# Kernel tuning notes

Hardware: AMD Instinct MI355X
Metric: run time of the kernel (lower is better)

The kernel has to match this reference:

```python
import jax, jax.numpy as jnp
import numpy as np

TOP_K = 2

def setup_inputs() -> dict:
    key = jax.random.key(0)
    k1, k2 = jax.random.split(key)
    x = jax.random.normal(k1, (4, 4096, 4096), dtype=jnp.float32)
    # nn.Linear(hidden, experts, bias=False) weight: [num_experts, hidden]
    gate_w = jax.random.normal(k2, (64, 4096), dtype=jnp.float32) * (1.0 / np.sqrt(4096.0))
    return {"x": x, "gate_w": gate_w}

def reference(x, gate_w):
    # logits: [b, s, e] = x @ gate_w.T
    logits = jnp.einsum('bsh,eh->bse', x, gate_w)
    top_k_logits, top_k_indices = jax.lax.top_k(logits, TOP_K)  # [b, s, k]
    # softmax over top-k logits in float32, cast back to logits dtype
    probs = jax.nn.softmax(top_k_logits.astype(jnp.float32), axis=-1).astype(logits.dtype)
    return (logits, top_k_indices, probs)
```

## Files before the change

kernel.cpp:

```cpp
#include <hip/hip_runtime.h>
#include <math.h>

#define H 4096
#define E 64
#define BMROWS 32
#define NT 256
#define KQ 1024
#define BK 32
#define NWIN (KQ / BK)

typedef short bf16x8 __attribute__((ext_vector_type(8)));
typedef float f32x4  __attribute__((ext_vector_type(4)));

__device__ __forceinline__ unsigned f2bf_rne_u(float f) {
    unsigned u = __float_as_uint(f);
    return (u + 0x7fffu + ((u >> 16) & 1u)) >> 16;
}

__global__ __launch_bounds__(256) void convert_w(const float* __restrict__ w,
                                                 unsigned short* __restrict__ wh,
                                                 unsigned short* __restrict__ wl) {
    const int i = (blockIdx.x * 256 + threadIdx.x) * 4;
    float4 v = *(const float4*)(w + i);
    float vv[4] = {v.x, v.y, v.z, v.w};
    unsigned hh[4], ll[4];
#pragma unroll
    for (int j = 0; j < 4; ++j) {
        hh[j] = f2bf_rne_u(vv[j]);
        float r = vv[j] - __uint_as_float(hh[j] << 16);
        ll[j] = __float_as_uint(r) >> 16;
    }
    ushort4 h, l;
    h.x = (unsigned short)hh[0]; h.y = (unsigned short)hh[1];
    h.z = (unsigned short)hh[2]; h.w = (unsigned short)hh[3];
    l.x = (unsigned short)ll[0]; l.y = (unsigned short)ll[1];
    l.z = (unsigned short)ll[2]; l.w = (unsigned short)ll[3];
    *(ushort4*)(wh + i) = h;
    *(ushort4*)(wl + i) = l;
}

__device__ __forceinline__ void cvt8(const float4 a, const float4 b,
                                     bf16x8& hi, bf16x8& lo) {
    float v[8] = {a.x, a.y, a.z, a.w, b.x, b.y, b.z, b.w};
#pragma unroll
    for (int i = 0; i < 8; ++i) {
        const unsigned u = __float_as_uint(v[i]);
        const unsigned t = u + 0x7fffu + ((u >> 16) & 1u);
        const float    r = v[i] - __uint_as_float(t & 0xffff0000u);
        hi[i] = (short)(t >> 16);
        lo[i] = (short)(__float_as_uint(r) >> 16);
    }
}

__global__ __launch_bounds__(NT, 2) void router_kernel(
    const float* __restrict__ x,
    const unsigned short* __restrict__ wh,
    const unsigned short* __restrict__ wl,
    float* __restrict__ out, int M)
{
    __shared__ __align__(16) f32x4 merge[8][4][64];

    const int t    = threadIdx.x;
    const int lane = t & 63;
    const int wk   = t >> 6;
    const int m0   = blockIdx.x * BMROWS;
    const int col  = lane & 15;
    const int quad = lane >> 4;

    const int kbase = wk * KQ + quad * 8;

    const float* xp0 = x + (size_t)(m0 + col) * H + kbase;
    const float* xp1 = x + (size_t)(m0 + 16 + col) * H + kbase;
    const unsigned short* whp = wh + (size_t)col * H + kbase;
    const unsigned short* wlp = wl + (size_t)col * H + kbase;

    f32x4 acc[2][4];
#pragma unroll
    for (int mt = 0; mt < 2; ++mt)
#pragma unroll
        for (int nt = 0; nt < 4; ++nt)
            acc[mt][nt] = (f32x4){0.0f, 0.0f, 0.0f, 0.0f};

    float4 x0[2][2], x1[2][2], x2[2][2], x3[2][2];
    uint4  wAh[4], wAl[4], wBh[4], wBl[4];

    auto loadx_into = [&](int win, float4 (&xb)[2][2]) {
        const int k = win * BK;
        xb[0][0] = *(const float4*)(xp0 + k);
        xb[0][1] = *(const float4*)(xp0 + k + 4);
        xb[1][0] = *(const float4*)(xp1 + k);
        xb[1][1] = *(const float4*)(xp1 + k + 4);
    };
    auto loadw_into = [&](int win, uint4 (&wh_)[4], uint4 (&wl_)[4]) {
        const int k = win * BK;
#pragma unroll
        for (int nt = 0; nt < 4; ++nt) {
            wh_[nt] = *(const uint4*)(whp + (size_t)(nt * 16) * H + k);
            wl_[nt] = *(const uint4*)(wlp + (size_t)(nt * 16) * H + k);
        }
    };

    auto step = [&](int win, float4 (&xc)[2][2], float4 (&xpref)[2][2],
                    uint4 (&whc)[4], uint4 (&wlc)[4],
                    uint4 (&whn)[4], uint4 (&wln)[4]) {
        if (win + 3 < NWIN) loadx_into(win + 3, xpref);
        if (win + 1 < NWIN) loadw_into(win + 1, whn, wln);
        bf16x8 ah[2], al[2];
        cvt8(xc[0][0], xc[0][1], ah[0], al[0]);
        cvt8(xc[1][0], xc[1][1], ah[1], al[1]);
#pragma unroll
        for (int nt = 0; nt < 4; ++nt) {
            const bf16x8 bh = __builtin_bit_cast(bf16x8, whc[nt]);
            const bf16x8 bl = __builtin_bit_cast(bf16x8, wlc[nt]);
#pragma unroll
            for (int mt = 0; mt < 2; ++mt) {
                acc[mt][nt] = __builtin_amdgcn_mfma_f32_16x16x32_bf16(
                    ah[mt], bh, acc[mt][nt], 0, 0, 0);
                acc[mt][nt] = __builtin_amdgcn_mfma_f32_16x16x32_bf16(
                    ah[mt], bl, acc[mt][nt], 0, 0, 0);
                acc[mt][nt] = __builtin_amdgcn_mfma_f32_16x16x32_bf16(
                    al[mt], bh, acc[mt][nt], 0, 0, 0);
            }
        }
    };

    loadx_into(0, x0);
    loadx_into(1, x1);
    loadx_into(2, x2);
    loadw_into(0, wAh, wAl);

#pragma unroll 1
    for (int win = 0; win < NWIN; win += 4) {
        step(win,     x0, x3, wAh, wAl, wBh, wBl);
        step(win + 1, x1, x0, wBh, wBl, wAh, wAl);
        step(win + 2, x2, x1, wAh, wAl, wBh, wBl);
        step(win + 3, x3, x2, wBh, wBl, wAh, wAl);
    }

#pragma unroll
    for (int mt = 0; mt < 2; ++mt)
#pragma unroll
        for (int nt = 0; nt < 4; ++nt)
            merge[mt * 4 + nt][wk][lane] = acc[mt][nt];
    __syncthreads();

    if (wk >= 2) return;
    const int mt = wk;

    f32x4 a2[4];
#pragma unroll
    for (int nt = 0; nt < 4; ++nt) {
        f32x4 s = merge[mt * 4 + nt][0][lane];
#pragma unroll
        for (int w = 1; w < 4; ++w)
            s += merge[mt * 4 + nt][w][lane];
        a2[nt] = s;
    }

    float* logits   = out;
    float* idx_out  = out + (size_t)M * E;
    float* prob_out = idx_out + (size_t)M * 2;

    const int mrow = m0 + mt * 16 + quad * 4;
#pragma unroll
    for (int r = 0; r < 4; ++r) {
#pragma unroll
        for (int nt = 0; nt < 4; ++nt)
            logits[(size_t)(mrow + r) * E + nt * 16 + col] = a2[nt][r];

        float v1 = a2[0][r], v2 = -INFINITY;
        int   i1 = col,      i2 = 0x7fffffff;
#pragma unroll
        for (int nt = 1; nt < 4; ++nt) {
            const float v = a2[nt][r];
            const int   e = nt * 16 + col;
            if (v > v1)      { v2 = v1; i2 = i1; v1 = v; i1 = e; }
            else if (v > v2) { v2 = v;  i2 = e; }
        }
#pragma unroll
        for (int mask = 1; mask < 16; mask <<= 1) {
            const float ov1 = __shfl_xor(v1, mask);
            const float ov2 = __shfl_xor(v2, mask);
            const int   oi1 = __shfl_xor(i1, mask);
            const int   oi2 = __shfl_xor(i2, mask);
            const bool afirst = (v1 > ov1) || (v1 == ov1 && i1 < oi1);
            float nv1, nv2; int ni1, ni2;
            if (afirst) {
                nv1 = v1; ni1 = i1;
                const bool s = (v2 > ov1) || (v2 == ov1 && i2 < oi1);
                nv2 = s ? v2 : ov1; ni2 = s ? i2 : oi1;
            } else {
                nv1 = ov1; ni1 = oi1;
                const bool s = (ov2 > v1) || (ov2 == v1 && oi2 < i1);
                nv2 = s ? ov2 : v1; ni2 = s ? oi2 : i1;
            }
            v1 = nv1; v2 = nv2; i1 = ni1; i2 = ni2;
        }
        if (col == 0) {
            const int m = mrow + r;
            const float e2 = __expf(v2 - v1);
            const float d  = 1.0f + e2;
            *(float2*)(idx_out  + (size_t)m * 2) = make_float2((float)i1, (float)i2);
            *(float2*)(prob_out + (size_t)m * 2) = make_float2(1.0f / d, e2 / d);
        }
    }
}

extern "C" void kernel_launch(void* const* d_in, const int* in_sizes, int n_in,
                              void* d_out, int out_size, void* d_ws, size_t ws_size,
                              hipStream_t stream) {
    const float* x = (const float*)d_in[0];
    const float* w = (const float*)d_in[1];
    unsigned short* wh = (unsigned short*)d_ws;
    unsigned short* wl = wh + (size_t)E * H;
    const int M = in_sizes[0] / H;

    hipLaunchKernelGGL(convert_w, dim3((E * H) / 1024), dim3(256), 0, stream,
                       w, wh, wl);
    hipLaunchKernelGGL(router_kernel, dim3(M / BMROWS), dim3(NT), 0, stream,
                       x, wh, wl, (float*)d_out, M);
}
```

Measured before the change: 403.4 us.

## Halve rows per block and drop weight double-buffering to raise occupancy

Each block now handles 16 rows instead of 32, with one M-tile per wave. The weight register double-buffer is replaced by a single buffer loaded at the start of each step, and launch bounds are raised to 4 blocks per SIMD group. This cuts register pressure and doubles the grid to raise occupancy and hide memory latency. In exchange, each weight fetch is reused by half as many rows, so weight traffic from L2 doubles, and weight loads are no longer prefetched one window ahead.

```diff
diff --git a/kernel.cpp b/kernel.cpp
--- a/kernel.cpp
+++ b/kernel.cpp
@@ -3,7 +3,7 @@
 
 #define H 4096
 #define E 64
-#define BMROWS 32
+#define BMROWS 16
 #define NT 256
 #define KQ 1024
 #define BK 32
@@ -52,13 +52,13 @@
     }
 }
 
-__global__ __launch_bounds__(NT, 2) void router_kernel(
+__global__ __launch_bounds__(NT, 4) void router_kernel(
     const float* __restrict__ x,
     const unsigned short* __restrict__ wh,
     const unsigned short* __restrict__ wl,
     float* __restrict__ out, int M)
 {
-    __shared__ __align__(16) f32x4 merge[8][4][64];
+    __shared__ __align__(16) f32x4 merge[4][4][64];
 
     const int t    = threadIdx.x;
     const int lane = t & 63;
@@ -69,91 +69,73 @@
 
     const int kbase = wk * KQ + quad * 8;
 
-    const float* xp0 = x + (size_t)(m0 + col) * H + kbase;
-    const float* xp1 = x + (size_t)(m0 + 16 + col) * H + kbase;
+    const float* xp = x + (size_t)(m0 + col) * H + kbase;
     const unsigned short* whp = wh + (size_t)col * H + kbase;
     const unsigned short* wlp = wl + (size_t)col * H + kbase;
 
-    f32x4 acc[2][4];
-#pragma unroll
-    for (int mt = 0; mt < 2; ++mt)
-#pragma unroll
-        for (int nt = 0; nt < 4; ++nt)
-            acc[mt][nt] = (f32x4){0.0f, 0.0f, 0.0f, 0.0f};
-
-    float4 x0[2][2], x1[2][2], x2[2][2], x3[2][2];
-    uint4  wAh[4], wAl[4], wBh[4], wBl[4];
-
-    auto loadx_into = [&](int win, float4 (&xb)[2][2]) {
+    f32x4 acc[4];
+#pragma unroll
+    for (int nt = 0; nt < 4; ++nt)
+        acc[nt] = (f32x4){0.0f, 0.0f, 0.0f, 0.0f};
+
+    float4 x0[2], x1[2], x2[2], x3[2];
+    uint4  wr[8];
+
+    auto loadx_into = [&](int win, float4 (&xb)[2]) {
         const int k = win * BK;
-        xb[0][0] = *(const float4*)(xp0 + k);
-        xb[0][1] = *(const float4*)(xp0 + k + 4);
-        xb[1][0] = *(const float4*)(xp1 + k);
-        xb[1][1] = *(const float4*)(xp1 + k + 4);
+        xb[0] = *(const float4*)(xp + k);
+        xb[1] = *(const float4*)(xp + k + 4);
     };
-    auto loadw_into = [&](int win, uint4 (&wh_)[4], uint4 (&wl_)[4]) {
+    auto loadw = [&](int win) {
         const int k = win * BK;
 #pragma unroll
         for (int nt = 0; nt < 4; ++nt) {
-            wh_[nt] = *(const uint4*)(whp + (size_t)(nt * 16) * H + k);
-            wl_[nt] = *(const uint4*)(wlp + (size_t)(nt * 16) * H + k);
+            wr[nt]     = *(const uint4*)(whp + (size_t)(nt * 16) * H + k);
+            wr[nt + 4] = *(const uint4*)(wlp + (size_t)(nt * 16) * H + k);
         }
     };
 
-    auto step = [&](int win, float4 (&xc)[2][2], float4 (&xpref)[2][2],
-                    uint4 (&whc)[4], uint4 (&wlc)[4],
-                    uint4 (&whn)[4], uint4 (&wln)[4]) {
+    auto step = [&](int win, float4 (&xc)[2], float4 (&xpref)[2]) {
+        loadw(win);
         if (win + 3 < NWIN) loadx_into(win + 3, xpref);
-        if (win + 1 < NWIN) loadw_into(win + 1, whn, wln);
-        bf16x8 ah[2], al[2];
-        cvt8(xc[0][0], xc[0][1], ah[0], al[0]);
-        cvt8(xc[1][0], xc[1][1], ah[1], al[1]);
+        bf16x8 ah, al;
+        cvt8(xc[0], xc[1], ah, al);
 #pragma unroll
         for (int nt = 0; nt < 4; ++nt) {
-            const bf16x8 bh = __builtin_bit_cast(bf16x8, whc[nt]);
-            const bf16x8 bl = __builtin_bit_cast(bf16x8, wlc[nt]);
-#pragma unroll
-            for (int mt = 0; mt < 2; ++mt) {
-                acc[mt][nt] = __builtin_amdgcn_mfma_f32_16x16x32_bf16(
-                    ah[mt], bh, acc[mt][nt], 0, 0, 0);
-                acc[mt][nt] = __builtin_amdgcn_mfma_f32_16x16x32_bf16(
-                    ah[mt], bl, acc[mt][nt], 0, 0, 0);
-                acc[mt][nt] = __builtin_amdgcn_mfma_f32_16x16x32_bf16(
-                    al[mt], bh, acc[mt][nt], 0, 0, 0);
-            }
+            const bf16x8 bh = __builtin_bit_cast(bf16x8, wr[nt]);
+            const bf16x8 bl = __builtin_bit_cast(bf16x8, wr[nt + 4]);
+            acc[nt] = __builtin_amdgcn_mfma_f32_16x16x32_bf16(ah, bh, acc[nt], 0, 0, 0);
+            acc[nt] = __builtin_amdgcn_mfma_f32_16x16x32_bf16(ah, bl, acc[nt], 0, 0, 0);
+            acc[nt] = __builtin_amdgcn_mfma_f32_16x16x32_bf16(al, bh, acc[nt], 0, 0, 0);
         }
     };
 
     loadx_into(0, x0);
     loadx_into(1, x1);
     loadx_into(2, x2);
-    loadw_into(0, wAh, wAl);
 
 #pragma unroll 1
     for (int win = 0; win < NWIN; win += 4) {
-        step(win,     x0, x3, wAh, wAl, wBh, wBl);
-        step(win + 1, x1, x0, wBh, wBl, wAh, wAl);
-        step(win + 2, x2, x1, wAh, wAl, wBh, wBl);
-        step(win + 3, x3, x2, wBh, wBl, wAh, wAl);
-    }
-
-#pragma unroll
-    for (int mt = 0; mt < 2; ++mt)
-#pragma unroll
-        for (int nt = 0; nt < 4; ++nt)
-            merge[mt * 4 + nt][wk][lane] = acc[mt][nt];
+        step(win,     x0, x3);
+        step(win + 1, x1, x0);
+        step(win + 2, x2, x1);
+        step(win + 3, x3, x2);
+    }
+
+#pragma unroll
+    for (int nt = 0; nt < 4; ++nt)
+        merge[nt][wk][lane] = acc[nt];
     __syncthreads();
 
-    if (wk >= 2) return;
-    const int mt = wk;
+    if (wk != 0) return;
 
     f32x4 a2[4];
 #pragma unroll
     for (int nt = 0; nt < 4; ++nt) {
-        f32x4 s = merge[mt * 4 + nt][0][lane];
+        f32x4 s = acc[nt];
 #pragma unroll
         for (int w = 1; w < 4; ++w)
-            s += merge[mt * 4 + nt][w][lane];
+            s += merge[nt][w][lane];
         a2[nt] = s;
     }
 
@@ -161,7 +143,7 @@
     float* idx_out  = out + (size_t)M * E;
     float* prob_out = idx_out + (size_t)M * 2;
 
-    const int mrow = m0 + mt * 16 + quad * 4;
+    const int mrow = m0 + quad * 4;
 #pragma unroll
     for (int r = 0; r < 4; ++r) {
 #pragma unroll
```

Result: slower. 453.4 us (+12.4%).

## Stage x tiles into LDS via direct global-to-LDS loads with triple buffering

Applied to the files above, without the earlier changes.

Activation tiles now go straight from global memory into shared memory through global_load_lds, into a triple-buffered, XOR-swizzled layout. Each wave reads them back from LDS, while weights stay in double-buffered registers. Hand-placed vmcnt waits and scheduling barriers control the pipeline depth. The aim is better-coalesced x loads (8 rows of 128 contiguous bytes per instruction), lower register pressure and more memory-level parallelism. The cost is reliance on exact vmcnt accounting, plus extra LDS traffic and shared-memory footprint.

```diff
diff --git a/kernel.cpp b/kernel.cpp
--- a/kernel.cpp
+++ b/kernel.cpp
@@ -12,6 +12,9 @@
 typedef short bf16x8 __attribute__((ext_vector_type(8)));
 typedef float f32x4  __attribute__((ext_vector_type(4)));
 
+#define GLBP(p) ((const __attribute__((address_space(1))) void*)(p))
+#define LDSP(p) ((__attribute__((address_space(3))) void*)(p))
+
 __device__ __forceinline__ unsigned f2bf_rne_u(float f) {
     unsigned u = __float_as_uint(f);
     return (u + 0x7fffu + ((u >> 16) & 1u)) >> 16;
@@ -39,9 +42,9 @@
     *(ushort4*)(wl + i) = l;
 }
 
-__device__ __forceinline__ void cvt8(const float4 a, const float4 b,
+__device__ __forceinline__ void cvt8(const f32x4 a, const f32x4 b,
                                      bf16x8& hi, bf16x8& lo) {
-    float v[8] = {a.x, a.y, a.z, a.w, b.x, b.y, b.z, b.w};
+    float v[8] = {a[0], a[1], a[2], a[3], b[0], b[1], b[2], b[3]};
 #pragma unroll
     for (int i = 0; i < 8; ++i) {
         const unsigned u = __float_as_uint(v[i]);
@@ -58,7 +61,7 @@
     const unsigned short* __restrict__ wl,
     float* __restrict__ out, int M)
 {
-    __shared__ __align__(16) f32x4 merge[8][4][64];
+    __shared__ __align__(16) float smem[3 * 4 * 1024];
 
     const int t    = threadIdx.x;
     const int lane = t & 63;
@@ -67,12 +70,18 @@
     const int col  = lane & 15;
     const int quad = lane >> 4;
 
-    const int kbase = wk * KQ + quad * 8;
-
-    const float* xp0 = x + (size_t)(m0 + col) * H + kbase;
-    const float* xp1 = x + (size_t)(m0 + 16 + col) * H + kbase;
-    const unsigned short* whp = wh + (size_t)col * H + kbase;
-    const unsigned short* wlp = wl + (size_t)col * H + kbase;
+    const int srow = lane >> 3;
+    const int scg  = (lane & 7) ^ srow;
+    const float* gx = x + (size_t)(m0 + srow) * H + wk * KQ + scg * 4;
+
+    const int r7 = col & 7;
+    const int sl00 = (col     ) * 8 + ((2 * quad    ) ^ r7);
+    const int sl01 = (col     ) * 8 + ((2 * quad + 1) ^ r7);
+    const int sl10 = (col + 16) * 8 + ((2 * quad    ) ^ r7);
+    const int sl11 = (col + 16) * 8 + ((2 * quad + 1) ^ r7);
+
+    const unsigned short* whp = wh + (size_t)col * H + wk * KQ + quad * 8;
+    const unsigned short* wlp = wl + (size_t)col * H + wk * KQ + quad * 8;
 
     f32x4 acc[2][4];
 #pragma unroll
@@ -81,37 +90,35 @@
         for (int nt = 0; nt < 4; ++nt)
             acc[mt][nt] = (f32x4){0.0f, 0.0f, 0.0f, 0.0f};
 
-    float4 x0[2][2], x1[2][2], x2[2][2], x3[2][2];
-    uint4  wAh[4], wAl[4], wBh[4], wBl[4];
-
-    auto loadx_into = [&](int win, float4 (&xb)[2][2]) {
-        const int k = win * BK;
-        xb[0][0] = *(const float4*)(xp0 + k);
-        xb[0][1] = *(const float4*)(xp0 + k + 4);
-        xb[1][0] = *(const float4*)(xp1 + k);
-        xb[1][1] = *(const float4*)(xp1 + k + 4);
+    uint4 wrA[8], wrB[8];
+
+    auto stage = [&](int win, int b) {
+        float* l = smem + (b * 4 + wk) * 1024;
+        const float* g = gx + (size_t)win * BK;
+#pragma unroll
+        for (int j = 0; j < 4; ++j)
+            __builtin_amdgcn_global_load_lds(GLBP(g + (size_t)j * 8 * H),
+                                             LDSP(l + j * 256), 16, 0, 0);
     };
-    auto loadw_into = [&](int win, uint4 (&wh_)[4], uint4 (&wl_)[4]) {
-        const int k = win * BK;
+    auto loadw = [&](int win, uint4 (&wr)[8]) {
+        const size_t k = (size_t)win * BK;
 #pragma unroll
         for (int nt = 0; nt < 4; ++nt) {
-            wh_[nt] = *(const uint4*)(whp + (size_t)(nt * 16) * H + k);
-            wl_[nt] = *(const uint4*)(wlp + (size_t)(nt * 16) * H + k);
+            wr[nt]     = *(const uint4*)(whp + (size_t)nt * 16 * H + k);
+            wr[nt + 4] = *(const uint4*)(wlp + (size_t)nt * 16 * H + k);
         }
     };
-
-    auto step = [&](int win, float4 (&xc)[2][2], float4 (&xpref)[2][2],
-                    uint4 (&whc)[4], uint4 (&wlc)[4],
-                    uint4 (&whn)[4], uint4 (&wln)[4]) {
-        if (win + 3 < NWIN) loadx_into(win + 3, xpref);
-        if (win + 1 < NWIN) loadw_into(win + 1, whn, wln);
+    auto compute = [&](int b, const uint4 (&wr)[8]) {
+        const f32x4* sv = (const f32x4*)smem + (size_t)(b * 4 + wk) * 256;
+        const f32x4 c00 = sv[sl00], c01 = sv[sl01];
+        const f32x4 c10 = sv[sl10], c11 = sv[sl11];
         bf16x8 ah[2], al[2];
-        cvt8(xc[0][0], xc[0][1], ah[0], al[0]);
-        cvt8(xc[1][0], xc[1][1], ah[1], al[1]);
+        cvt8(c00, c01, ah[0], al[0]);
+        cvt8(c10, c11, ah[1], al[1]);
 #pragma unroll
         for (int nt = 0; nt < 4; ++nt) {
-            const bf16x8 bh = __builtin_bit_cast(bf16x8, whc[nt]);
-            const bf16x8 bl = __builtin_bit_cast(bf16x8, wlc[nt]);
+            const bf16x8 bh = __builtin_bit_cast(bf16x8, wr[nt]);
+            const bf16x8 bl = __builtin_bit_cast(bf16x8, wr[nt + 4]);
 #pragma unroll
             for (int mt = 0; mt < 2; ++mt) {
                 acc[mt][nt] = __builtin_amdgcn_mfma_f32_16x16x32_bf16(
@@ -124,24 +131,42 @@
         }
     };
 
-    loadx_into(0, x0);
-    loadx_into(1, x1);
-    loadx_into(2, x2);
-    loadw_into(0, wAh, wAl);
-
+    stage(0, 0);
+    stage(1, 1);
+    __builtin_amdgcn_sched_barrier(0);
+    loadw(0, wrA);
+
+    int b = 0;
 #pragma unroll 1
-    for (int win = 0; win < NWIN; win += 4) {
-        step(win,     x0, x3, wAh, wAl, wBh, wBl);
-        step(win + 1, x1, x0, wBh, wBl, wAh, wAl);
-        step(win + 2, x2, x1, wAh, wAl, wBh, wBl);
-        step(win + 3, x3, x2, wBh, wBl, wAh, wAl);
-    }
-
+    for (int win = 0; win < NWIN; win += 2) {
+        asm volatile("s_waitcnt vmcnt(12)" ::: "memory");
+        __builtin_amdgcn_sched_barrier(0);
+        {
+            int b2 = b + 2; if (b2 >= 3) b2 -= 3;
+            if (win + 2 < NWIN) stage(win + 2, b2);
+            __builtin_amdgcn_sched_barrier(0);
+            if (win + 1 < NWIN) loadw(win + 1, wrB);
+            compute(b, wrA);
+        }
+        asm volatile("s_waitcnt vmcnt(12)" ::: "memory");
+        __builtin_amdgcn_sched_barrier(0);
+        {
+            int b1 = b + 1; if (b1 >= 3) b1 -= 3;
+            if (win + 3 < NWIN) stage(win + 3, b);
+            __builtin_amdgcn_sched_barrier(0);
+            if (win + 2 < NWIN) loadw(win + 2, wrA);
+            compute(b1, wrB);
+        }
+        b = (b + 2 >= 3) ? b - 1 : b + 2;
+    }
+
+    __syncthreads();
+    f32x4* mg = (f32x4*)smem;
 #pragma unroll
     for (int mt = 0; mt < 2; ++mt)
 #pragma unroll
         for (int nt = 0; nt < 4; ++nt)
-            merge[mt * 4 + nt][wk][lane] = acc[mt][nt];
+            mg[(size_t)(mt * 4 + nt) * 256 + wk * 64 + lane] = acc[mt][nt];
     __syncthreads();
 
     if (wk >= 2) return;
@@ -150,10 +175,10 @@
     f32x4 a2[4];
 #pragma unroll
     for (int nt = 0; nt < 4; ++nt) {
-        f32x4 s = merge[mt * 4 + nt][0][lane];
+        f32x4 s = mg[(size_t)(mt * 4 + nt) * 256 + lane];
 #pragma unroll
         for (int w = 1; w < 4; ++w)
-            s += merge[mt * 4 + nt][w][lane];
+            s += mg[(size_t)(mt * 4 + nt) * 256 + w * 64 + lane];
         a2[nt] = s;
     }
 
```

Result: no change. 402.0 us (-0.3%).
